# Kernel tuning notes

Measured on AMD Instinct MI355X. Metric: run time of the kernel, lower is better.

## Reference

```python
import jax, jax.numpy as jnp
import numpy as np

N_HEAD, D_K, D_V, D_MODEL = 16, 64, 64, 1024
LN_EPS = 1e-5


def setup_inputs() -> dict:
    key = jax.random.key(0)
    ks = jax.random.split(key, 13)
    B, S = 2, 2048
    s = 1.0 / np.sqrt(D_MODEL)
    return {
        "q": jax.random.normal(ks[0], (B, S, D_MODEL), jnp.float32),
        "k": jax.random.normal(ks[1], (B, S, D_MODEL), jnp.float32),
        "v": jax.random.normal(ks[2], (B, S, D_MODEL), jnp.float32),
        "Wq": jax.random.normal(ks[3], (D_MODEL, N_HEAD * D_K), jnp.float32) * s,
        "bq": jnp.zeros((N_HEAD * D_K,), jnp.float32),
        "Wk": jax.random.normal(ks[4], (D_MODEL, N_HEAD * D_K), jnp.float32) * s,
        "bk": jnp.zeros((N_HEAD * D_K,), jnp.float32),
        "Wv": jax.random.normal(ks[5], (D_MODEL, N_HEAD * D_V), jnp.float32) * s,
        "bv": jnp.zeros((N_HEAD * D_V,), jnp.float32),
        "Wo": jax.random.normal(ks[6], (N_HEAD * D_V, D_MODEL), jnp.float32) * s,
        "bo": jnp.zeros((D_MODEL,), jnp.float32),
        "ln_gamma": jnp.ones((D_MODEL,), jnp.float32),
        "ln_beta": jnp.zeros((D_MODEL,), jnp.float32),
    }


def reference(q, k, v, Wq, bq, Wk, bk, Wv, bv, Wo, bo, ln_gamma, ln_beta):
    B, S, _ = q.shape
    temperature = jnp.asarray(np.power(D_K, 0.5), q.dtype)
    # QKV projections -> [B, S, H, d]
    q_ = (q @ Wq + bq).reshape(B, S, N_HEAD, D_K)
    k_ = (k @ Wk + bk).reshape(B, S, N_HEAD, D_K)
    v_ = (v @ Wv + bv).reshape(B, S, N_HEAD, D_V)
    # scaled dot-product attention per head
    scores = jnp.einsum("bqhd,bkhd->bhqk", q_, k_) / temperature
    attn = jax.nn.softmax(scores, axis=-1)
    ctx = jnp.einsum("bhqk,bkhd->bqhd", attn, v_).reshape(B, S, N_HEAD * D_V)
    # output projection + residual + LayerNorm
    out = ctx @ Wo + bo + q
    mu = jnp.mean(out, axis=-1, keepdims=True)
    var = jnp.var(out, axis=-1, keepdims=True)
    out = (out - mu) * jax.lax.rsqrt(var + LN_EPS) * ln_gamma + ln_beta
    return out
```

## Files before the change

### kernel.cpp

```cpp
#include <hip/hip_runtime.h>
#include <hip/hip_bf16.h>

typedef float f32x4 __attribute__((ext_vector_type(4)));
typedef float f32x16 __attribute__((ext_vector_type(16)));
typedef __bf16 bf16x8 __attribute__((ext_vector_type(8)));
typedef __bf16 bf16x4 __attribute__((ext_vector_type(4)));
typedef unsigned u32x2 __attribute__((ext_vector_type(2)));

#define DM 1024
#define SL 2048
#define NHEAD 16
#define LOG2E 1.44269504088896f
#define EXP2(x) __builtin_amdgcn_exp2f(x)

static __device__ __forceinline__ f32x4 mfma16(bf16x8 a, bf16x8 b, f32x4 c) {
    return __builtin_amdgcn_mfma_f32_16x16x32_bf16(a, b, c, 0, 0, 0);
}
static __device__ __forceinline__ f32x16 mfma32(bf16x8 a, bf16x8 b, f32x16 c) {
    return __builtin_amdgcn_mfma_f32_32x32x16_bf16(a, b, c, 0, 0, 0);
}

static __device__ __forceinline__ void gload16(const void* g, void* l) {
    __builtin_amdgcn_global_load_lds(
        (const __attribute__((address_space(1))) unsigned*)g,
        (__attribute__((address_space(3))) unsigned*)l, 16, 0, 0);
}

static __device__ __forceinline__ unsigned packbf(float lo, float hi) {
    unsigned short lu = __builtin_bit_cast(unsigned short, (__bf16)lo);
    unsigned short hu = __builtin_bit_cast(unsigned short, (__bf16)hi);
    return ((unsigned)hu << 16) | (unsigned)lu;
}

__global__ __launch_bounds__(256) void prep_kernel(
    const float* __restrict__ x0, const float* __restrict__ x1, const float* __restrict__ x2,
    __bf16* __restrict__ y0, __bf16* __restrict__ y1, __bf16* __restrict__ y2,
    const float* __restrict__ W0, const float* __restrict__ W1,
    const float* __restrict__ W2, const float* __restrict__ W3,
    __bf16* __restrict__ T0, __bf16* __restrict__ T1,
    __bf16* __restrict__ T2, __bf16* __restrict__ T3)
{
    const int bid = blockIdx.x;
    if (bid < 6144) {
        const int yy = bid >> 11, xx = bid & 2047;
        const float* x = (yy == 0) ? x0 : (yy == 1) ? x1 : x2;
        __bf16* y = (yy == 0) ? y0 : (yy == 1) ? y1 : y2;
        size_t i = ((size_t)xx * 256 + threadIdx.x) * 8;
        float4 a = *reinterpret_cast<const float4*>(&x[i]);
        float4 b = *reinterpret_cast<const float4*>(&x[i + 4]);
        bf16x8 o;
        o[0] = (__bf16)a.x; o[1] = (__bf16)a.y; o[2] = (__bf16)a.z; o[3] = (__bf16)a.w;
        o[4] = (__bf16)b.x; o[5] = (__bf16)b.y; o[6] = (__bf16)b.z; o[7] = (__bf16)b.w;
        *reinterpret_cast<bf16x8*>(&y[i]) = o;
    } else {
        __shared__ float tle[32][33];
        const int rem = bid - 6144;
        const int z = rem >> 10, r2 = rem & 1023;
        const int bx = r2 & 31, by = r2 >> 5;
        const float* W = (z == 0) ? W0 : (z == 1) ? W1 : (z == 2) ? W2 : W3;
        __bf16* Wt = (z == 0) ? T0 : (z == 1) ? T1 : (z == 2) ? T2 : T3;
        const int tx = threadIdx.x & 31, ty = threadIdx.x >> 5;
        const int n0 = bx * 32, k0 = by * 32;
#pragma unroll
        for (int i = 0; i < 4; ++i) {
            int r = ty + 8 * i;
            tle[r][tx] = W[(size_t)(k0 + r) * DM + (n0 + tx)];
        }
        __syncthreads();
#pragma unroll
        for (int i = 0; i < 4; ++i) {
            int r = ty + 8 * i;
            Wt[(size_t)(n0 + r) * DM + (k0 + tx)] = (__bf16)tle[tx][r];
        }
    }
}

static __device__ __forceinline__ void gemm64_body(
    const __bf16* __restrict__ A, const __bf16* __restrict__ Wt,
    const float* __restrict__ bias, const float* __restrict__ resid,
    __bf16* __restrict__ Yb, float* __restrict__ Yf,
    int mode, float oscale, int r0, int c0)
{
    __shared__ __attribute__((aligned(16))) __bf16 As[128 * 64];
    __shared__ __attribute__((aligned(16))) __bf16 Bs[64 * 64];
    const int t = threadIdx.x;
    const int w = t >> 6, lane = t & 63;
    const int l15 = lane & 15, lhi = lane >> 4;
    const int wr = w >> 1, wc = w & 1;
    const int lrow = lane >> 3;
    const int lcolswz = (((lane & 7) ^ lrow) << 3);
    const int jb = w * 4, jb2 = w * 2;
    const int swzr = (l15 & 7) << 3;

    const f32x4 fzero = {0.f, 0.f, 0.f, 0.f};
    f32x4 acc[4][2];
#pragma unroll
    for (int m = 0; m < 4; ++m)
#pragma unroll
        for (int n = 0; n < 2; ++n) acc[m][n] = fzero;

    const __bf16* gA = &A[(size_t)(r0 + jb * 8 + lrow) * DM + lcolswz];
    const __bf16* gB = &Wt[(size_t)(c0 + jb2 * 8 + lrow) * DM + lcolswz];

    for (int kt = 0; kt < DM; kt += 64) {
        __syncthreads();
#pragma unroll
        for (int i = 0; i < 4; ++i)
            gload16(gA + (size_t)i * 8 * DM + kt, &As[(jb + i) * 512]);
#pragma unroll
        for (int i = 0; i < 2; ++i)
            gload16(gB + (size_t)i * 8 * DM + kt, &Bs[(jb2 + i) * 512]);
        __syncthreads();
#pragma unroll
        for (int kk = 0; kk < 2; ++kk) {
            bf16x8 af[4], bfr[2];
#pragma unroll
            for (int m = 0; m < 4; ++m)
                af[m] = *reinterpret_cast<const bf16x8*>(
                    &As[(wr * 64 + m * 16 + l15) * 64 + ((kk * 32 + lhi * 8) ^ swzr)]);
#pragma unroll
            for (int n = 0; n < 2; ++n)
                bfr[n] = *reinterpret_cast<const bf16x8*>(
                    &Bs[(wc * 32 + n * 16 + l15) * 64 + ((kk * 32 + lhi * 8) ^ swzr)]);
#pragma unroll
            for (int m = 0; m < 4; ++m)
#pragma unroll
                for (int n = 0; n < 2; ++n)
                    acc[m][n] = mfma16(af[m], bfr[n], acc[m][n]);
        }
    }
    if (mode == 0) {
#pragma unroll
        for (int m = 0; m < 4; ++m)
#pragma unroll
            for (int n = 0; n < 2; ++n)
#pragma unroll
                for (int r = 0; r < 4; ++r) {
                    int grow = r0 + wr * 64 + m * 16 + lhi * 4 + r;
                    int gcol = c0 + wc * 32 + n * 16 + l15;
                    Yb[(size_t)grow * DM + gcol] =
                        (__bf16)((acc[m][n][r] + bias[gcol]) * oscale);
                }
    } else if (mode == 1) {
#pragma unroll
        for (int m = 0; m < 4; ++m)
#pragma unroll
            for (int n = 0; n < 2; ++n) {
                int token = r0 + wr * 64 + m * 16 + lhi * 4;
                int gcol = c0 + wc * 32 + n * 16 + l15;
                int bb = token >> 11, ss = token & (SL - 1);
                int hh = gcol >> 6, dd = gcol & 63;
                float bv = bias[gcol];
                bf16x4 pv;
#pragma unroll
                for (int r = 0; r < 4; ++r) pv[r] = (__bf16)(acc[m][n][r] + bv);
                *reinterpret_cast<bf16x4*>(
                    &Yb[(((size_t)(bb * NHEAD + hh)) * 64 + dd) * SL + ss]) = pv;
            }
    } else {
#pragma unroll
        for (int m = 0; m < 4; ++m)
#pragma unroll
            for (int n = 0; n < 2; ++n)
#pragma unroll
                for (int r = 0; r < 4; ++r) {
                    int grow = r0 + wr * 64 + m * 16 + lhi * 4 + r;
                    int gcol = c0 + wc * 32 + n * 16 + l15;
                    size_t idx = (size_t)grow * DM + gcol;
                    Yf[idx] = acc[m][n][r] + bias[gcol] + resid[idx];
                }
    }
}

__global__ __launch_bounds__(256) void qkv_kernel(
    const __bf16* __restrict__ xq, const __bf16* __restrict__ xk, const __bf16* __restrict__ xv,
    const __bf16* __restrict__ WtQ, const __bf16* __restrict__ WtK, const __bf16* __restrict__ WtV,
    const float* __restrict__ bq, const float* __restrict__ bk, const float* __restrict__ bv,
    __bf16* __restrict__ Qp, __bf16* __restrict__ Kp, __bf16* __restrict__ Vt)
{
    const int p = blockIdx.x;
    const int logical = (p & 7) * 192 + (p >> 3);
    const int x = logical & 15;
    const int s = logical >> 4;
    const int y = s & 31, z = s >> 5;
    const __bf16* X = (z == 0) ? xq : (z == 1) ? xk : xv;
    const __bf16* Wt = (z == 0) ? WtQ : (z == 1) ? WtK : WtV;
    const float* bias = (z == 0) ? bq : (z == 1) ? bk : bv;
    __bf16* Yb = (z == 0) ? Qp : (z == 1) ? Kp : Vt;
    int mode = (z == 2) ? 1 : 0;
    float oscale = (z == 0) ? (0.125f * LOG2E) : 1.0f;
    gemm64_body(X, Wt, bias, nullptr, Yb, nullptr, mode, oscale, y * 128, x * 64);
}

__global__ __launch_bounds__(256) void oproj_kernel(
    const __bf16* __restrict__ Cxb, const __bf16* __restrict__ WtO,
    const float* __restrict__ bo, const float* __restrict__ resid,
    float* __restrict__ pre)
{
    const int p = blockIdx.x;
    const int logical = (p & 7) * 64 + (p >> 3);
    const int x = logical & 15, y = logical >> 4;
    gemm64_body(Cxb, WtO, bo, resid, nullptr, pre, 2, 1.0f, y * 128, x * 64);
}

__global__ __launch_bounds__(256, 4) void attn_kernel(
    const __bf16* __restrict__ Qp, const __bf16* __restrict__ Kp,
    const __bf16* __restrict__ Vt, __bf16* __restrict__ Op, float2* __restrict__ ML)
{
    __shared__ __attribute__((aligned(16))) __bf16 Kl[2][4096];
    __shared__ __attribute__((aligned(16))) __bf16 Vl[2][4096];
    const int t = threadIdx.x;
    const int w = t >> 6, lane = t & 63;
    const int l31 = lane & 31, hi = lane >> 5;

    const int id = blockIdx.x;
    const int logical = (id & 7) * 128 + (id >> 3);
    const int bh = logical >> 5, rr = logical & 31;
    const int qs = rr >> 1, half = rr & 1;
    const int b = bh >> 4, h = bh & 15;
    const size_t tokQ = (size_t)b * SL + qs * 128 + w * 32;
    const size_t kbase = (size_t)b * SL + half * 1024;
    const size_t vrow0 = (size_t)bh * 64;

    const int srow = t >> 3, scol = (t & 7) << 3;
    const __bf16* gK = &Kp[(kbase + srow) * DM + h * 64 + scol];
    const __bf16* gV = &Vt[(vrow0 + srow) * SL + half * 1024 + scol];
    const int sidxA = ((srow * 128 + scol * 2) ^ ((srow & 7) << 4)) >> 1;
    const int sidxB = sidxA + 2048;

    bf16x8 bq[4];
#pragma unroll
    for (int ks = 0; ks < 4; ++ks)
        bq[ks] = *reinterpret_cast<const bf16x8*>(
            &Qp[(tokQ + l31) * DM + h * 64 + ks * 16 + hi * 8]);

    f32x16 o0, o1;
#pragma unroll
    for (int r = 0; r < 16; ++r) { o0[r] = 0.f; o1[r] = 0.f; }
    float m_run = -1e30f, l_run = 0.f;

    const int swz = (l31 & 7) << 4;
    const int NT = 1024 / 64;

    {
        *reinterpret_cast<bf16x8*>(&Kl[0][sidxA]) = *reinterpret_cast<const bf16x8*>(gK);
        *reinterpret_cast<bf16x8*>(&Kl[0][sidxB]) = *reinterpret_cast<const bf16x8*>(gK + (size_t)32 * DM);
        *reinterpret_cast<bf16x8*>(&Vl[0][sidxA]) = *reinterpret_cast<const bf16x8*>(gV);
        *reinterpret_cast<bf16x8*>(&Vl[0][sidxB]) = *reinterpret_cast<const bf16x8*>(gV + (size_t)32 * SL);
    }

    for (int ti = 0; ti < NT; ++ti) {
        const int cb = ti & 1;
        const bool pf = (ti + 1 < NT);
        bf16x8 kvnA, kvnB, vvnA, vvnB;
        if (pf) {
            const __bf16* nK = gK + (size_t)(ti + 1) * 64 * DM;
            const __bf16* nV = gV + (ti + 1) * 64;
            kvnA = *reinterpret_cast<const bf16x8*>(nK);
            kvnB = *reinterpret_cast<const bf16x8*>(nK + (size_t)32 * DM);
            vvnA = *reinterpret_cast<const bf16x8*>(nV);
            vvnB = *reinterpret_cast<const bf16x8*>(nV + (size_t)32 * SL);
        }
        __syncthreads();

        f32x16 c0, c1;
#pragma unroll
        for (int r = 0; r < 16; ++r) { c0[r] = 0.f; c1[r] = 0.f; }
        __builtin_amdgcn_s_setprio(1);
#pragma unroll
        for (int ks = 0; ks < 4; ++ks) {
            int off = ks * 32 + hi * 16;
            bf16x8 ak0 = *reinterpret_cast<const bf16x8*>(&Kl[cb][((l31 * 128 + off) ^ swz) >> 1]);
            bf16x8 ak1 = *reinterpret_cast<const bf16x8*>(&Kl[cb][(((32 + l31) * 128 + off) ^ swz) >> 1]);
            c0 = mfma32(ak0, bq[ks], c0);
            c1 = mfma32(ak1, bq[ks], c1);
        }
        __builtin_amdgcn_s_setprio(0);

        float mx[8];
#pragma unroll
        for (int r = 0; r < 8; ++r)
            mx[r] = fmaxf(fmaxf(c0[r], c0[r + 8]), fmaxf(c1[r], c1[r + 8]));
#pragma unroll
        for (int r = 0; r < 4; ++r) mx[r] = fmaxf(mx[r], mx[r + 4]);
        float tm = fmaxf(fmaxf(mx[0], mx[1]), fmaxf(mx[2], mx[3]));
        tm = fmaxf(tm, __shfl_xor(tm, 32));

        if (__any(tm > m_run + 11.5f)) {
            float nm = fmaxf(m_run, tm);
            float sc = EXP2(m_run - nm);
            m_run = nm;
            l_run *= sc;
#pragma unroll
            for (int r = 0; r < 16; ++r) {
                float sq = __shfl(sc, (r & 3) + 8 * (r >> 2) + 4 * hi);
                o0[r] *= sq; o1[r] *= sq;
            }
        }

        float s4a = 0.f, s4b = 0.f, s4c = 0.f, s4d = 0.f;
#pragma unroll
        for (int r = 0; r < 16; r += 4) {
            c0[r]     = EXP2(c0[r]     - m_run); s4a += c0[r];
            c0[r + 1] = EXP2(c0[r + 1] - m_run); s4b += c0[r + 1];
            c0[r + 2] = EXP2(c0[r + 2] - m_run); s4c += c0[r + 2];
            c0[r + 3] = EXP2(c0[r + 3] - m_run); s4d += c0[r + 3];
        }
#pragma unroll
        for (int r = 0; r < 16; r += 4) {
            c1[r]     = EXP2(c1[r]     - m_run); s4a += c1[r];
            c1[r + 1] = EXP2(c1[r + 1] - m_run); s4b += c1[r + 1];
            c1[r + 2] = EXP2(c1[r + 2] - m_run); s4c += c1[r + 2];
            c1[r + 3] = EXP2(c1[r + 3] - m_run); s4d += c1[r + 3];
        }
        float rs = (s4a + s4b) + (s4c + s4d);
        rs += __shfl_xor(rs, 32);
        l_run += rs;

        if (pf) {
            *reinterpret_cast<bf16x8*>(&Kl[cb ^ 1][sidxA]) = kvnA;
            *reinterpret_cast<bf16x8*>(&Kl[cb ^ 1][sidxB]) = kvnB;
            *reinterpret_cast<bf16x8*>(&Vl[cb ^ 1][sidxA]) = vvnA;
            *reinterpret_cast<bf16x8*>(&Vl[cb ^ 1][sidxB]) = vvnB;
        }

        unsigned wd0[8], wd1[8];
#pragma unroll
        for (int tt = 0; tt < 4; ++tt)
#pragma unroll
            for (int p = 0; p < 2; ++p) {
                wd0[tt * 2 + p] = packbf(c0[4 * tt + 2 * p], c0[4 * tt + 2 * p + 1]);
                wd1[tt * 2 + p] = packbf(c1[4 * tt + 2 * p], c1[4 * tt + 2 * p + 1]);
            }
        unsigned ua[4][4];
#pragma unroll
        for (int s = 0; s < 4; ++s) {
            int tA = (s & 1) * 2;
#pragma unroll
            for (int p = 0; p < 2; ++p) {
                unsigned va = (s < 2) ? wd0[tA * 2 + p] : wd1[tA * 2 + p];
                unsigned vb = (s < 2) ? wd0[(tA + 1) * 2 + p] : wd1[(tA + 1) * 2 + p];
                u32x2 rres = __builtin_amdgcn_permlane32_swap(va, vb, false, false);
                ua[s][p] = rres[0]; ua[s][2 + p] = rres[1];
            }
        }

        __builtin_amdgcn_s_setprio(1);
#pragma unroll
        for (int s = 0; s < 4; ++s) {
            bf16x8 as = *reinterpret_cast<const bf16x8*>(&ua[s][0]);
            bf16x8 vf0 = *reinterpret_cast<const bf16x8*>(
                &Vl[cb][((l31 * 128 + s * 32 + hi * 16) ^ swz) >> 1]);
            bf16x8 vf1 = *reinterpret_cast<const bf16x8*>(
                &Vl[cb][(((32 + l31) * 128 + s * 32 + hi * 16) ^ swz) >> 1]);
            o0 = mfma32(as, vf0, o0);
            o1 = mfma32(as, vf1, o1);
        }
        __builtin_amdgcn_s_setprio(0);
    }

    if (hi == 0)
        ML[((size_t)half * 4096 + tokQ + l31) * NHEAD + h] = float2{m_run, l_run};
    const size_t obase = (size_t)half * 4096 * DM;
#pragma unroll
    for (int r = 0; r < 16; ++r) {
        int qq = (r & 3) + 8 * (r >> 2) + 4 * hi;
        size_t rowi = obase + (tokQ + qq) * DM + h * 64;
        Op[rowi + l31]      = (__bf16)o0[r];
        Op[rowi + 32 + l31] = (__bf16)o1[r];
    }
}

__global__ __launch_bounds__(256) void combine_kernel(
    const __bf16* __restrict__ Op, const float2* __restrict__ ML,
    __bf16* __restrict__ Cxb)
{
    const size_t e = ((size_t)blockIdx.x * 256 + threadIdx.x) * 8;
    const int token = (int)(e >> 10);
    const int h = (int)((e >> 6) & 15);
    float2 ml0 = ML[(size_t)token * NHEAD + h];
    float2 ml1 = ML[((size_t)4096 + token) * NHEAD + h];
    float M = fmaxf(ml0.x, ml1.x);
    float s0 = EXP2(ml0.x - M), s1 = EXP2(ml1.x - M);
    float inv = 1.f / (ml0.y * s0 + ml1.y * s1);
    s0 *= inv; s1 *= inv;
    bf16x8 a0 = *reinterpret_cast<const bf16x8*>(&Op[e]);
    bf16x8 a1 = *reinterpret_cast<const bf16x8*>(&Op[(size_t)4096 * DM + e]);
    bf16x8 o;
#pragma unroll
    for (int j = 0; j < 8; ++j)
        o[j] = (__bf16)((float)a0[j] * s0 + (float)a1[j] * s1);
    *reinterpret_cast<bf16x8*>(&Cxb[e]) = o;
}

__global__ __launch_bounds__(256) void ln_kernel(
    const float* __restrict__ X, const float* __restrict__ gamma,
    const float* __restrict__ beta, float* __restrict__ out)
{
    const int row = blockIdx.x, t = threadIdx.x;
    float4 v = *reinterpret_cast<const float4*>(&X[(size_t)row * DM + t * 4]);
    float s = v.x + v.y + v.z + v.w;
    float s2 = v.x * v.x + v.y * v.y + v.z * v.z + v.w * v.w;
#pragma unroll
    for (int off = 1; off < 64; off <<= 1) {
        s += __shfl_xor(s, off);
        s2 += __shfl_xor(s2, off);
    }
    __shared__ float rs[4], rs2[4];
    const int w = t >> 6;
    if ((t & 63) == 0) { rs[w] = s; rs2[w] = s2; }
    __syncthreads();
    s = rs[0] + rs[1] + rs[2] + rs[3];
    s2 = rs2[0] + rs2[1] + rs2[2] + rs2[3];
    float mean = s * (1.f / DM);
    float var = s2 * (1.f / DM) - mean * mean;
    float rstd = rsqrtf(var + 1e-5f);
    int c = t * 4;
    float4 o;
    o.x = (v.x - mean) * rstd * gamma[c + 0] + beta[c + 0];
    o.y = (v.y - mean) * rstd * gamma[c + 1] + beta[c + 1];
    o.z = (v.z - mean) * rstd * gamma[c + 2] + beta[c + 2];
    o.w = (v.w - mean) * rstd * gamma[c + 3] + beta[c + 3];
    *reinterpret_cast<float4*>(&out[(size_t)row * DM + c]) = o;
}

extern "C" void kernel_launch(void* const* d_in, const int* in_sizes, int n_in,
                              void* d_out, int out_size, void* d_ws, size_t ws_size,
                              hipStream_t stream) {
    (void)in_sizes; (void)n_in; (void)out_size; (void)ws_size;
    const float* q   = (const float*)d_in[0];
    const float* k   = (const float*)d_in[1];
    const float* v   = (const float*)d_in[2];
    const float* Wq  = (const float*)d_in[3];
    const float* bq  = (const float*)d_in[4];
    const float* Wk  = (const float*)d_in[5];
    const float* bk  = (const float*)d_in[6];
    const float* Wv  = (const float*)d_in[7];
    const float* bv  = (const float*)d_in[8];
    const float* Wo  = (const float*)d_in[9];
    const float* bo  = (const float*)d_in[10];
    const float* lng = (const float*)d_in[11];
    const float* lnb = (const float*)d_in[12];

    char* ws = (char*)d_ws;
    const size_t MB = (size_t)1 << 20;
    __bf16* WtQ = (__bf16*)(ws + 0 * MB);
    __bf16* WtK = (__bf16*)(ws + 2 * MB);
    __bf16* WtV = (__bf16*)(ws + 4 * MB);
    __bf16* WtO = (__bf16*)(ws + 6 * MB);
    __bf16* Xbq = (__bf16*)(ws + 8 * MB);
    __bf16* Xbk = (__bf16*)(ws + 16 * MB);
    __bf16* Xbv = (__bf16*)(ws + 24 * MB);
    __bf16* Qp  = (__bf16*)(ws + 32 * MB);
    __bf16* Kp  = (__bf16*)(ws + 40 * MB);
    __bf16* Vt  = (__bf16*)(ws + 48 * MB);
    __bf16* Cxb = (__bf16*)(ws + 56 * MB);
    __bf16* Op  = (__bf16*)(ws + 8 * MB);
    float2* ML  = (float2*)(ws + 24 * MB);
    float*  pre = (float*)(ws + 8 * MB);

    prep_kernel<<<dim3(10240), 256, 0, stream>>>(q, k, v, Xbq, Xbk, Xbv,
                                                 Wq, Wk, Wv, Wo, WtQ, WtK, WtV, WtO);

    qkv_kernel<<<dim3(1536), 256, 0, stream>>>(Xbq, Xbk, Xbv, WtQ, WtK, WtV,
                                               bq, bk, bv, Qp, Kp, Vt);
    attn_kernel<<<dim3(1024), 256, 0, stream>>>(Qp, Kp, Vt, Op, ML);
    combine_kernel<<<dim3(2048), 256, 0, stream>>>(Op, ML, Cxb);
    oproj_kernel<<<dim3(512), 256, 0, stream>>>(Cxb, WtO, bo, q, pre);
    ln_kernel<<<4096, 256, 0, stream>>>(pre, lng, lnb, (float*)d_out);
}
```

Before: 146.1 us.

## Widen attention blocks to 256 queries and split KV three ways

The attention kernel now runs 512 threads (8 waves) per block covering 256 query rows. Each K/V tile loaded into LDS is therefore shared by twice as many queries, and each thread stages one 16-byte chunk per tile instead of two. The KV range is split into three uneven partitions (10/11/11 tiles) instead of two halves, giving a 768-block grid. The combine kernel merges three partial results with their max/sum statistics, and the ML buffer moves to the region freed by the Q weights. The aim is to cut global and LDS traffic per query and improve grid fill on the CUs. The cost is more partial-output traffic in combine, uneven work across partitions, and tighter register limits from the larger launch bounds.

```diff
diff --git a/kernel.cpp b/kernel.cpp
--- a/kernel.cpp
+++ b/kernel.cpp
@@ -203,7 +203,7 @@
     gemm64_body(Cxb, WtO, bo, resid, nullptr, pre, 2, 1.0f, y * 128, x * 64);
 }
 
-__global__ __launch_bounds__(256, 4) void attn_kernel(
+__global__ __launch_bounds__(512, 4) void attn_kernel(
     const __bf16* __restrict__ Qp, const __bf16* __restrict__ Kp,
     const __bf16* __restrict__ Vt, __bf16* __restrict__ Op, float2* __restrict__ ML)
 {
@@ -214,19 +214,20 @@
     const int l31 = lane & 31, hi = lane >> 5;
 
     const int id = blockIdx.x;
-    const int logical = (id & 7) * 128 + (id >> 3);
-    const int bh = logical >> 5, rr = logical & 31;
-    const int qs = rr >> 1, half = rr & 1;
+    const int logical = (id & 7) * 96 + (id >> 3);
+    const int part = logical >> 8;
+    const int rem = logical & 255;
+    const int bh = rem >> 3, qs = rem & 7;
     const int b = bh >> 4, h = bh & 15;
-    const size_t tokQ = (size_t)b * SL + qs * 128 + w * 32;
-    const size_t kbase = (size_t)b * SL + half * 1024;
+    const int t0 = (part * 32) / 3, t1 = ((part + 1) * 32) / 3;
+    const size_t tokQ = (size_t)b * SL + qs * 256 + w * 32;
+    const size_t kbase = (size_t)b * SL;
     const size_t vrow0 = (size_t)bh * 64;
 
     const int srow = t >> 3, scol = (t & 7) << 3;
     const __bf16* gK = &Kp[(kbase + srow) * DM + h * 64 + scol];
-    const __bf16* gV = &Vt[(vrow0 + srow) * SL + half * 1024 + scol];
-    const int sidxA = ((srow * 128 + scol * 2) ^ ((srow & 7) << 4)) >> 1;
-    const int sidxB = sidxA + 2048;
+    const __bf16* gV = &Vt[(vrow0 + srow) * SL + scol];
+    const int sidx = ((srow * 128 + scol * 2) ^ ((srow & 7) << 4)) >> 1;
 
     bf16x8 bq[4];
 #pragma unroll
@@ -240,26 +241,21 @@
     float m_run = -1e30f, l_run = 0.f;
 
     const int swz = (l31 & 7) << 4;
-    const int NT = 1024 / 64;
 
     {
-        *reinterpret_cast<bf16x8*>(&Kl[0][sidxA]) = *reinterpret_cast<const bf16x8*>(gK);
-        *reinterpret_cast<bf16x8*>(&Kl[0][sidxB]) = *reinterpret_cast<const bf16x8*>(gK + (size_t)32 * DM);
-        *reinterpret_cast<bf16x8*>(&Vl[0][sidxA]) = *reinterpret_cast<const bf16x8*>(gV);
-        *reinterpret_cast<bf16x8*>(&Vl[0][sidxB]) = *reinterpret_cast<const bf16x8*>(gV + (size_t)32 * SL);
-    }
-
-    for (int ti = 0; ti < NT; ++ti) {
-        const int cb = ti & 1;
-        const bool pf = (ti + 1 < NT);
-        bf16x8 kvnA, kvnB, vvnA, vvnB;
+        bf16x8 kv = *reinterpret_cast<const bf16x8*>(gK + (size_t)t0 * 64 * DM);
+        bf16x8 vv = *reinterpret_cast<const bf16x8*>(gV + t0 * 64);
+        *reinterpret_cast<bf16x8*>(&Kl[0][sidx]) = kv;
+        *reinterpret_cast<bf16x8*>(&Vl[0][sidx]) = vv;
+    }
+
+    for (int ti = t0; ti < t1; ++ti) {
+        const int cb = (ti - t0) & 1;
+        const bool pf = (ti + 1 < t1);
+        bf16x8 kvn, vvn;
         if (pf) {
-            const __bf16* nK = gK + (size_t)(ti + 1) * 64 * DM;
-            const __bf16* nV = gV + (ti + 1) * 64;
-            kvnA = *reinterpret_cast<const bf16x8*>(nK);
-            kvnB = *reinterpret_cast<const bf16x8*>(nK + (size_t)32 * DM);
-            vvnA = *reinterpret_cast<const bf16x8*>(nV);
-            vvnB = *reinterpret_cast<const bf16x8*>(nV + (size_t)32 * SL);
+            kvn = *reinterpret_cast<const bf16x8*>(gK + (size_t)(ti + 1) * 64 * DM);
+            vvn = *reinterpret_cast<const bf16x8*>(gV + (ti + 1) * 64);
         }
         __syncthreads();
 
@@ -318,10 +314,8 @@
         l_run += rs;
 
         if (pf) {
-            *reinterpret_cast<bf16x8*>(&Kl[cb ^ 1][sidxA]) = kvnA;
-            *reinterpret_cast<bf16x8*>(&Kl[cb ^ 1][sidxB]) = kvnB;
-            *reinterpret_cast<bf16x8*>(&Vl[cb ^ 1][sidxA]) = vvnA;
-            *reinterpret_cast<bf16x8*>(&Vl[cb ^ 1][sidxB]) = vvnB;
+            *reinterpret_cast<bf16x8*>(&Kl[cb ^ 1][sidx]) = kvn;
+            *reinterpret_cast<bf16x8*>(&Vl[cb ^ 1][sidx]) = vvn;
         }
 
         unsigned wd0[8], wd1[8];
@@ -360,8 +354,8 @@
     }
 
     if (hi == 0)
-        ML[((size_t)half * 4096 + tokQ + l31) * NHEAD + h] = float2{m_run, l_run};
-    const size_t obase = (size_t)half * 4096 * DM;
+        ML[((size_t)part * 4096 + tokQ + l31) * NHEAD + h] = float2{m_run, l_run};
+    const size_t obase = (size_t)part * 4096 * DM;
 #pragma unroll
     for (int r = 0; r < 16; ++r) {
         int qq = (r & 3) + 8 * (r >> 2) + 4 * hi;
@@ -380,16 +374,18 @@
     const int h = (int)((e >> 6) & 15);
     float2 ml0 = ML[(size_t)token * NHEAD + h];
     float2 ml1 = ML[((size_t)4096 + token) * NHEAD + h];
-    float M = fmaxf(ml0.x, ml1.x);
-    float s0 = EXP2(ml0.x - M), s1 = EXP2(ml1.x - M);
-    float inv = 1.f / (ml0.y * s0 + ml1.y * s1);
-    s0 *= inv; s1 *= inv;
+    float2 ml2 = ML[((size_t)8192 + token) * NHEAD + h];
+    float M = fmaxf(fmaxf(ml0.x, ml1.x), ml2.x);
+    float s0 = EXP2(ml0.x - M), s1 = EXP2(ml1.x - M), s2 = EXP2(ml2.x - M);
+    float inv = 1.f / (ml0.y * s0 + ml1.y * s1 + ml2.y * s2);
+    s0 *= inv; s1 *= inv; s2 *= inv;
     bf16x8 a0 = *reinterpret_cast<const bf16x8*>(&Op[e]);
     bf16x8 a1 = *reinterpret_cast<const bf16x8*>(&Op[(size_t)4096 * DM + e]);
+    bf16x8 a2 = *reinterpret_cast<const bf16x8*>(&Op[(size_t)8192 * DM + e]);
     bf16x8 o;
 #pragma unroll
     for (int j = 0; j < 8; ++j)
-        o[j] = (__bf16)((float)a0[j] * s0 + (float)a1[j] * s1);
+        o[j] = (__bf16)((float)a0[j] * s0 + (float)a1[j] * s1 + (float)a2[j] * s2);
     *reinterpret_cast<bf16x8*>(&Cxb[e]) = o;
 }
 
@@ -455,8 +451,8 @@
     __bf16* Kp  = (__bf16*)(ws + 40 * MB);
     __bf16* Vt  = (__bf16*)(ws + 48 * MB);
     __bf16* Cxb = (__bf16*)(ws + 56 * MB);
+    float2* ML  = (float2*)(ws + 0 * MB);
     __bf16* Op  = (__bf16*)(ws + 8 * MB);
-    float2* ML  = (float2*)(ws + 24 * MB);
     float*  pre = (float*)(ws + 8 * MB);
 
     prep_kernel<<<dim3(10240), 256, 0, stream>>>(q, k, v, Xbq, Xbk, Xbv,
@@ -464,7 +460,7 @@
 
     qkv_kernel<<<dim3(1536), 256, 0, stream>>>(Xbq, Xbk, Xbv, WtQ, WtK, WtV,
                                                bq, bk, bv, Qp, Kp, Vt);
-    attn_kernel<<<dim3(1024), 256, 0, stream>>>(Qp, Kp, Vt, Op, ML);
+    attn_kernel<<<dim3(768), 512, 0, stream>>>(Qp, Kp, Vt, Op, ML);
     combine_kernel<<<dim3(2048), 256, 0, stream>>>(Op, ML, Cxb);
     oproj_kernel<<<dim3(512), 256, 0, stream>>>(Cxb, WtO, bo, q, pre);
     ln_kernel<<<4096, 256, 0, stream>>>(pre, lng, lnb, (float*)d_out);
```

Result: faster. 141.0 us (-3.5%).
